# Performance work log

Measured on AMD Instinct MI355X. Metric: run time of the kernel, lower is better.

Reference implementation:

```python
import jax, jax.numpy as jnp
import numpy as np

N_HEAD = 16
D_MODEL = 1024
HEAD_DIM = D_MODEL // N_HEAD
B, S = 2, 2048


def setup_inputs() -> dict:
    key = jax.random.key(0)
    ks = jax.random.split(key, 7)
    qry = jax.random.normal(ks[0], (B, S, D_MODEL), dtype=jnp.float32)
    k_in = jax.random.normal(ks[1], (B, S, D_MODEL), dtype=jnp.float32)
    v_in = jax.random.normal(ks[2], (B, S, D_MODEL), dtype=jnp.float32)
    # causal boolean mask (B, S_q, S_k) as asserted in SelfAttention.forward
    attn_mask = jnp.broadcast_to(jnp.tril(jnp.ones((S, S), dtype=bool)), (B, S, S))
    scale = 1.0 / np.sqrt(D_MODEL)
    Wq = jax.random.normal(ks[3], (D_MODEL, D_MODEL), dtype=jnp.float32) * scale
    Wk = jax.random.normal(ks[4], (D_MODEL, D_MODEL), dtype=jnp.float32) * scale
    Wv = jax.random.normal(ks[5], (D_MODEL, D_MODEL), dtype=jnp.float32) * scale
    Wo = jax.random.normal(ks[6], (D_MODEL, D_MODEL), dtype=jnp.float32) * scale
    return {"qry": qry, "key": k_in, "val": v_in, "attn_mask": attn_mask,
            "Wq": Wq, "Wk": Wk, "Wv": Wv, "Wo": Wo}


def reference(qry, key, val, attn_mask, Wq, Wk, Wv, Wo):
    Bq, Sq, _ = qry.shape
    # torch Linear: y = x @ W.T (no bias)
    q = (qry @ Wq.T).reshape(Bq, Sq, N_HEAD, HEAD_DIM).transpose(0, 2, 1, 3)
    k = (key @ Wk.T).reshape(Bq, -1, N_HEAD, HEAD_DIM).transpose(0, 2, 1, 3)
    v = (val @ Wv.T).reshape(Bq, -1, N_HEAD, HEAD_DIM).transpose(0, 2, 1, 3)
    # scores: [B, H, Sq, Sk]
    scores = jnp.einsum('bhqd,bhkd->bhqk', q, k) / jnp.sqrt(jnp.float32(HEAD_DIM * N_HEAD) / N_HEAD)
    # attn_bias: 0 where mask True, -inf where False; broadcast over heads
    bias = jnp.where(attn_mask[:, None, :, :], 0.0, -jnp.inf).astype(scores.dtype)
    attn_weights = jax.nn.softmax(scores + bias, axis=-1)
    attn_feats = jnp.einsum('bhqk,bhkd->bhqd', attn_weights, v)
    attn_feats = attn_feats.transpose(0, 2, 1, 3).reshape(Bq, Sq, D_MODEL)
    output = attn_feats @ Wo.T
    return output, attn_weights
```

## Files before the change

### kernel.cpp

```cpp
#include <hip/hip_runtime.h>
#include <hip/hip_bf16.h>
#include <cstdint>
#include <cstddef>

#define DM 1024
#define NH 16
#define HD 64
#define BB 2
#define SS 2048

typedef __attribute__((ext_vector_type(4))) float f32x4;
typedef __attribute__((ext_vector_type(8))) short bf16x8;

typedef __attribute__((address_space(1))) const void GV;
typedef __attribute__((address_space(3))) void LV;

__global__ __launch_bounds__(256) void cvt_all(
    const float* s0, const float* s1, const float* s2, const float* s3,
    const float* s4, const float* s5, const float* s6,
    __hip_bfloat16* d0, __hip_bfloat16* d1, __hip_bfloat16* d2, __hip_bfloat16* d3,
    __hip_bfloat16* d4, __hip_bfloat16* d5, __hip_bfloat16* d6) {
    const float* s; __hip_bfloat16* d; int n4;
    switch (blockIdx.y) {
        case 0: s = s0; d = d0; n4 = 1 << 20; break;
        case 1: s = s1; d = d1; n4 = 1 << 20; break;
        case 2: s = s2; d = d2; n4 = 1 << 20; break;
        case 3: s = s3; d = d3; n4 = 1 << 18; break;
        case 4: s = s4; d = d4; n4 = 1 << 18; break;
        case 5: s = s5; d = d5; n4 = 1 << 18; break;
        default: s = s6; d = d6; n4 = 1 << 18; break;
    }
    for (int i = blockIdx.x * 256 + threadIdx.x; i < n4; i += 1024 * 256) {
        float4 v = reinterpret_cast<const float4*>(s)[i];
        ushort4 o;
        o.x = __builtin_bit_cast(unsigned short, __float2bfloat16(v.x));
        o.y = __builtin_bit_cast(unsigned short, __float2bfloat16(v.y));
        o.z = __builtin_bit_cast(unsigned short, __float2bfloat16(v.z));
        o.w = __builtin_bit_cast(unsigned short, __float2bfloat16(v.w));
        reinterpret_cast<ushort4*>(d)[i] = o;
    }
}

template <typename OutT>
__device__ __forceinline__ void gemm_body(const __hip_bfloat16* __restrict__ A,
                                          const __hip_bfloat16* __restrict__ Bw,
                                          OutT* __restrict__ C, int M, int N, int K,
                                          float alpha,
                                          __hip_bfloat16* As, __hip_bfloat16* Bs) {
    const int lane = threadIdx.x & 63;
    const int wv = threadIdx.x >> 6;
    const int wr = wv >> 1, wc = wv & 1;
    const int g = lane >> 4, cq = lane & 15;
    const int tM = blockIdx.y * 128, tN = blockIdx.x * 128;

    f32x4 acc[4][4];
#pragma unroll
    for (int i = 0; i < 4; ++i)
#pragma unroll
        for (int j = 0; j < 4; ++j) acc[i][j] = (f32x4){0.f, 0.f, 0.f, 0.f};

    for (int k0 = 0; k0 < K; k0 += 32) {
        __syncthreads();
#pragma unroll
        for (int r = 0; r < 2; ++r) {
            int chunk = r * 256 + wv * 64 + lane;
            int row = chunk >> 2;
            int kk = (chunk & 3) * 8;
            __builtin_amdgcn_global_load_lds((GV*)(A + (size_t)(tM + row) * K + k0 + kk),
                                             (LV*)(As + (size_t)(r * 256 + wv * 64) * 8), 16, 0, 0);
            __builtin_amdgcn_global_load_lds((GV*)(Bw + (size_t)(tN + row) * K + k0 + kk),
                                             (LV*)(Bs + (size_t)(r * 256 + wv * 64) * 8), 16, 0, 0);
        }
        __syncthreads();

        bf16x8 af[4], bfr[4];
#pragma unroll
        for (int i = 0; i < 4; ++i)
            af[i] = *reinterpret_cast<const bf16x8*>(As + (wr * 64 + i * 16 + cq) * 32 + g * 8);
#pragma unroll
        for (int j = 0; j < 4; ++j)
            bfr[j] = *reinterpret_cast<const bf16x8*>(Bs + (wc * 64 + j * 16 + cq) * 32 + g * 8);
#pragma unroll
        for (int i = 0; i < 4; ++i)
#pragma unroll
            for (int j = 0; j < 4; ++j)
                acc[i][j] = __builtin_amdgcn_mfma_f32_16x16x32_bf16(af[i], bfr[j], acc[i][j], 0, 0, 0);
    }

#pragma unroll
    for (int i = 0; i < 4; ++i)
#pragma unroll
        for (int j = 0; j < 4; ++j)
#pragma unroll
            for (int rr = 0; rr < 4; ++rr) {
                int row = tM + wr * 64 + i * 16 + g * 4 + rr;
                int col = tN + wc * 64 + j * 16 + cq;
                float v = acc[i][j][rr] * alpha;
                if constexpr (__is_same(OutT, float)) {
                    C[(size_t)row * N + col] = v;
                } else {
                    C[(size_t)row * N + col] = __float2bfloat16(v);
                }
            }
}

#define QALPHA 0.1803368801111204f

__global__ __launch_bounds__(256) void gemm_qkv(
    const __hip_bfloat16* qa, const __hip_bfloat16* ka, const __hip_bfloat16* va,
    const __hip_bfloat16* wq, const __hip_bfloat16* wk, const __hip_bfloat16* wv,
    __hip_bfloat16* Qm, __hip_bfloat16* Km, __hip_bfloat16* Vm) {
    __shared__ __hip_bfloat16 As[128 * 32];
    __shared__ __hip_bfloat16 Bs[128 * 32];
    const __hip_bfloat16 *A, *Bw;
    __hip_bfloat16* C;
    float alpha = 1.0f;
    switch (blockIdx.z) {
        case 0: A = qa; Bw = wq; C = Qm; alpha = QALPHA; break;
        case 1: A = ka; Bw = wk; C = Km; break;
        default: A = va; Bw = wv; C = Vm; break;
    }
    gemm_body<__hip_bfloat16>(A, Bw, C, BB * SS, DM, DM, alpha, As, Bs);
}

__global__ __launch_bounds__(256) void gemm_out(const __hip_bfloat16* __restrict__ A,
                                                const __hip_bfloat16* __restrict__ Bw,
                                                float* __restrict__ C) {
    __shared__ __hip_bfloat16 As[128 * 32];
    __shared__ __hip_bfloat16 Bs[128 * 32];
    gemm_body<float>(A, Bw, C, BB * SS, DM, DM, 1.0f, As, Bs);
}

__global__ __launch_bounds__(256) void transpose_v(const __hip_bfloat16* __restrict__ V,
                                                   __hip_bfloat16* __restrict__ VT) {
    const int bh = blockIdx.x;
    const int b = bh >> 4, h = bh & 15;
    const int k0 = blockIdx.y * 64;
    __shared__ __hip_bfloat16 tile[64][65];
    const int r = threadIdx.x / 64;
    const int c = threadIdx.x % 64;
#pragma unroll
    for (int rr = r; rr < 64; rr += 4)
        tile[rr][c] = V[(size_t)(b * SS + k0 + rr) * DM + h * HD + c];
    __syncthreads();
#pragma unroll
    for (int rr = r; rr < 64; rr += 4)
        VT[((size_t)bh * HD + rr) * SS + k0 + c] = tile[c][rr];
}

__global__ __launch_bounds__(256) void attn_fused(const __hip_bfloat16* __restrict__ Q,
                                                  const __hip_bfloat16* __restrict__ Kb,
                                                  const __hip_bfloat16* __restrict__ VT,
                                                  float* __restrict__ Wout,
                                                  __hip_bfloat16* __restrict__ feats) {
    __shared__ __hip_bfloat16 klds[2][64][64];
    __shared__ __hip_bfloat16 vlds[2][64][64];
    __shared__ __hip_bfloat16 plds[4][16][64];
    const int qt = (SS / 64 - 1) - blockIdx.x;
    const int bh = blockIdx.y;
    const int b = bh >> 4, h = bh & 15;
    const int lane = threadIdx.x & 63;
    const int wv = threadIdx.x >> 6;
    const int g = lane >> 4, cq = lane & 15;
    const int q0w = qt * 64 + wv * 16;
    const size_t rowbase = (size_t)b * SS;
    const int tmaxw = q0w >> 4;

    const __hip_bfloat16* qp = Q + (rowbase + q0w + cq) * DM + h * HD + g * 8;
    const bf16x8 qf0 = *reinterpret_cast<const bf16x8*>(qp);
    const bf16x8 qf1 = *reinterpret_cast<const bf16x8*>(qp + 32);

    auto stageK = [&](int kc, int buf) {
#pragma unroll
        for (int i = 0; i < 2; ++i) {
            int slot = i * 256 + wv * 64 + lane;
            int row = slot >> 3, c16 = slot & 7;
            const __hip_bfloat16* src =
                Kb + (rowbase + kc * 64 + row) * DM + h * HD + ((c16 ^ (row & 7)) << 3);
            __builtin_amdgcn_global_load_lds(
                (GV*)src, (LV*)(&klds[buf][0][0] + (size_t)(i * 256 + wv * 64) * 8), 16, 0, 0);
        }
    };
    auto stageV = [&](int kc, int buf) {
#pragma unroll
        for (int i = 0; i < 2; ++i) {
            int slot = i * 256 + wv * 64 + lane;
            int row = slot >> 3, c16 = slot & 7;
            const __hip_bfloat16* src =
                VT + ((size_t)bh * HD + row) * SS + kc * 64 + ((c16 ^ (row & 7)) << 3);
            __builtin_amdgcn_global_load_lds(
                (GV*)src, (LV*)(&vlds[buf][0][0] + (size_t)(i * 256 + wv * 64) * 8), 16, 0, 0);
        }
    };

    const int swx = cq & 7;

    float l_[4] = {0.f, 0.f, 0.f, 0.f};
    stageK(0, 0);
    for (int kc = 0; kc <= qt; ++kc) {
        const int cur = kc & 1;
        __syncthreads();
        if (kc < qt) stageK(kc + 1, cur ^ 1);
#pragma unroll
        for (int hh = 0; hh < 4; ++hh) {
            const int kt = kc * 4 + hh;
            if (kt > tmaxw) break;
            const __hip_bfloat16* kb = &klds[cur][hh * 16 + cq][0];
            bf16x8 kf0 = *reinterpret_cast<const bf16x8*>(kb + ((g ^ swx) << 3));
            bf16x8 kf1 = *reinterpret_cast<const bf16x8*>(kb + (((4 + g) ^ swx) << 3));
            f32x4 sc = (f32x4){0.f, 0.f, 0.f, 0.f};
            sc = __builtin_amdgcn_mfma_f32_16x16x32_bf16(qf0, kf0, sc, 0, 0, 0);
            sc = __builtin_amdgcn_mfma_f32_16x16x32_bf16(qf1, kf1, sc, 0, 0, 0);
            const int kk = kt * 16 + cq;
#pragma unroll
            for (int r = 0; r < 4; ++r) {
                const int qr = q0w + g * 4 + r;
                float p = (kk <= qr) ? __builtin_amdgcn_exp2f(sc[r]) : 0.0f;
                l_[r] += p;
            }
        }
    }
    float invl[4];
#pragma unroll
    for (int r = 0; r < 4; ++r) {
        float l = l_[r];
#pragma unroll
        for (int mk = 1; mk < 16; mk <<= 1) l += __shfl_xor(l, mk);
        invl[r] = __builtin_amdgcn_rcpf(l);
    }

    f32x4 oacc[4];
#pragma unroll
    for (int j = 0; j < 4; ++j) oacc[j] = (f32x4){0.f, 0.f, 0.f, 0.f};

    __syncthreads();
    stageK(0, 0);
    stageV(0, 0);
    for (int kc = 0; kc <= qt; ++kc) {
        const int cur = kc & 1;
        __syncthreads();
        if (kc < qt) { stageK(kc + 1, cur ^ 1); stageV(kc + 1, cur ^ 1); }

#pragma unroll
        for (int hh = 0; hh < 4; ++hh) {
            const int kt = kc * 4 + hh;
            if (kt <= tmaxw) {
                const __hip_bfloat16* kb = &klds[cur][hh * 16 + cq][0];
                bf16x8 kf0 = *reinterpret_cast<const bf16x8*>(kb + ((g ^ swx) << 3));
                bf16x8 kf1 = *reinterpret_cast<const bf16x8*>(kb + (((4 + g) ^ swx) << 3));
                f32x4 sc = (f32x4){0.f, 0.f, 0.f, 0.f};
                sc = __builtin_amdgcn_mfma_f32_16x16x32_bf16(qf0, kf0, sc, 0, 0, 0);
                sc = __builtin_amdgcn_mfma_f32_16x16x32_bf16(qf1, kf1, sc, 0, 0, 0);
                const int kk = kt * 16 + cq;
#pragma unroll
                for (int r = 0; r < 4; ++r) {
                    const int row = g * 4 + r;
                    const int qr = q0w + row;
                    float w = (kk <= qr) ? __builtin_amdgcn_exp2f(sc[r]) * invl[r] : 0.0f;
                    plds[wv][row][(hh * 16 + cq) ^ (8 * (row & 7))] = __float2bfloat16(w);
                }
            } else {
#pragma unroll
                for (int r = 0; r < 4; ++r) {
                    const int row = g * 4 + r;
                    plds[wv][row][(hh * 16 + cq) ^ (8 * (row & 7))] = __float2bfloat16(0.0f);
                }
            }
        }

        const int sw = 8 * swx;
        bf16x8 wa0 = *reinterpret_cast<const bf16x8*>(&plds[wv][cq][(g * 8) ^ sw]);
        bf16x8 wa1 = *reinterpret_cast<const bf16x8*>(&plds[wv][cq][(32 + g * 8) ^ sw]);
        __builtin_amdgcn_s_setprio(1);
#pragma unroll
        for (int j = 0; j < 4; ++j) {
            const __hip_bfloat16* vb = &vlds[cur][j * 16 + cq][0];
            bf16x8 vb0 = *reinterpret_cast<const bf16x8*>(vb + ((g ^ swx) << 3));
            bf16x8 vb1 = *reinterpret_cast<const bf16x8*>(vb + (((4 + g) ^ swx) << 3));
            oacc[j] = __builtin_amdgcn_mfma_f32_16x16x32_bf16(wa0, vb0, oacc[j], 0, 0, 0);
            oacc[j] = __builtin_amdgcn_mfma_f32_16x16x32_bf16(wa1, vb1, oacc[j], 0, 0, 0);
        }
        __builtin_amdgcn_s_setprio(0);

#pragma unroll
        for (int rh = 0; rh < 2; ++rh)
#pragma unroll
            for (int ch = 0; ch < 2; ++ch) {
                const int row = rh * 8 + (lane >> 3);
                const int fc = ch * 32 + (lane & 7) * 4;
                ushort4 u = *reinterpret_cast<const ushort4*>(
                    &plds[wv][row][fc ^ (8 * (row & 7))]);
                f32x4 v4;
                v4[0] = __builtin_bit_cast(float, (uint32_t)u.x << 16);
                v4[1] = __builtin_bit_cast(float, (uint32_t)u.y << 16);
                v4[2] = __builtin_bit_cast(float, (uint32_t)u.z << 16);
                v4[3] = __builtin_bit_cast(float, (uint32_t)u.w << 16);
                __builtin_nontemporal_store(
                    v4, reinterpret_cast<f32x4*>(
                            Wout + ((size_t)bh * SS + q0w + row) * SS + kc * 64 + fc));
            }
    }

    const int zstart = (qt + 1) * 64;
    const f32x4 z4 = (f32x4){0.f, 0.f, 0.f, 0.f};
    const int zrow = lane >> 2;
    const int zc = (lane & 3) * 4;
    for (int c = zstart; c < SS; c += 64) {
#pragma unroll
        for (int it = 0; it < 4; ++it) {
            f32x4* p = reinterpret_cast<f32x4*>(
                Wout + ((size_t)bh * SS + q0w + zrow) * SS + c + it * 16 + zc);
            __builtin_nontemporal_store(z4, p);
        }
    }

#pragma unroll
    for (int j = 0; j < 4; ++j)
#pragma unroll
        for (int r = 0; r < 4; ++r)
            feats[(rowbase + q0w + g * 4 + r) * DM + h * HD + j * 16 + cq] =
                __float2bfloat16(oacc[j][r]);
}

extern "C" void kernel_launch(void* const* d_in, const int* in_sizes, int n_in,
                              void* d_out, int out_size, void* d_ws, size_t ws_size,
                              hipStream_t stream) {
    (void)in_sizes; (void)n_in; (void)out_size;
    const float* qry = (const float*)d_in[0];
    const float* key = (const float*)d_in[1];
    const float* val = (const float*)d_in[2];
    const float* Wq = (const float*)d_in[4];
    const float* Wk = (const float*)d_in[5];
    const float* Wv = (const float*)d_in[6];
    const float* Wo = (const float*)d_in[7];

    float* out = (float*)d_out;
    float* w_out = out + (size_t)BB * SS * DM;

    const size_t E = (size_t)BB * SS * DM;
    const size_t W = (size_t)DM * DM;
    if (ws_size < (8 * E + 4 * W) * sizeof(__hip_bfloat16)) return;

    __hip_bfloat16* ws = (__hip_bfloat16*)d_ws;
    __hip_bfloat16* qb    = ws;
    __hip_bfloat16* kb    = ws + E;
    __hip_bfloat16* vb    = ws + 2 * E;
    __hip_bfloat16* wqb   = ws + 3 * E;
    __hip_bfloat16* wkb   = ws + 3 * E + W;
    __hip_bfloat16* wvb   = ws + 3 * E + 2 * W;
    __hip_bfloat16* wob   = ws + 3 * E + 3 * W;
    __hip_bfloat16* Qm    = ws + 3 * E + 4 * W;
    __hip_bfloat16* Km    = ws + 4 * E + 4 * W;
    __hip_bfloat16* Vm    = ws + 5 * E + 4 * W;
    __hip_bfloat16* VTm   = ws + 6 * E + 4 * W;
    __hip_bfloat16* feats = ws + 7 * E + 4 * W;

    cvt_all<<<dim3(1024, 7), 256, 0, stream>>>(qry, key, val, Wq, Wk, Wv, Wo,
                                               qb, kb, vb, wqb, wkb, wvb, wob);

    gemm_qkv<<<dim3(DM / 128, (BB * SS) / 128, 3), 256, 0, stream>>>(
        qb, kb, vb, wqb, wkb, wvb, Qm, Km, Vm);

    transpose_v<<<dim3(BB * NH, SS / 64), 256, 0, stream>>>(Vm, VTm);

    attn_fused<<<dim3(SS / 64, BB * NH), 256, 0, stream>>>(Qm, Km, VTm, w_out, feats);

    gemm_out<<<dim3(DM / 128, (BB * SS) / 128), 256, 0, stream>>>(feats, wob, out);
}
```

Measured before the change: 284.5 us.

## Fuse V transpose into QKV GEMM epilogue and restructure attention weight writes

The V projection GEMM now writes its output directly in transposed per-head layout, which removes the separate transpose kernel and its extra round trip through global memory. The attention kernel swaps the MFMA operands so that each lane holds four consecutive key scores for one query row. This lets the probabilities go straight from registers to the fp32 weight output as vector stores instead of being bounced through LDS, and it cuts the row-sum reduction to two shuffles. The launch becomes a 1D grid with a remapped order that spreads heavy causal tiles across blocks, and bf16 packing now uses v_cvt_pk_bf16_f32. The tradeoff is that the epilogue stores in the V GEMM become scattered, and the weight stores are 16-byte per lane rather than fully coalesced rows.

```diff
diff --git a/kernel.cpp b/kernel.cpp
--- a/kernel.cpp
+++ b/kernel.cpp
@@ -11,9 +11,16 @@
 
 typedef __attribute__((ext_vector_type(4))) float f32x4;
 typedef __attribute__((ext_vector_type(8))) short bf16x8;
+typedef __attribute__((ext_vector_type(2))) unsigned int u32x2;
 
 typedef __attribute__((address_space(1))) const void GV;
 typedef __attribute__((address_space(3))) void LV;
+
+__device__ __forceinline__ uint32_t cvtpk_bf16(float lo, float hi) {
+    uint32_t r;
+    asm("v_cvt_pk_bf16_f32 %0, %1, %2" : "=v"(r) : "v"(lo), "v"(hi));
+    return r;
+}
 
 __global__ __launch_bounds__(256) void cvt_all(
     const float* s0, const float* s1, const float* s2, const float* s3,
@@ -41,11 +48,10 @@
     }
 }
 
-template <typename OutT>
+template <int MODE>
 __device__ __forceinline__ void gemm_body(const __hip_bfloat16* __restrict__ A,
                                           const __hip_bfloat16* __restrict__ Bw,
-                                          OutT* __restrict__ C, int M, int N, int K,
-                                          float alpha,
+                                          void* __restrict__ Cv, float alpha,
                                           __hip_bfloat16* As, __hip_bfloat16* Bs) {
     const int lane = threadIdx.x & 63;
     const int wv = threadIdx.x >> 6;
@@ -59,16 +65,16 @@
 #pragma unroll
         for (int j = 0; j < 4; ++j) acc[i][j] = (f32x4){0.f, 0.f, 0.f, 0.f};
 
-    for (int k0 = 0; k0 < K; k0 += 32) {
+    for (int k0 = 0; k0 < DM; k0 += 32) {
         __syncthreads();
 #pragma unroll
         for (int r = 0; r < 2; ++r) {
             int chunk = r * 256 + wv * 64 + lane;
             int row = chunk >> 2;
             int kk = (chunk & 3) * 8;
-            __builtin_amdgcn_global_load_lds((GV*)(A + (size_t)(tM + row) * K + k0 + kk),
+            __builtin_amdgcn_global_load_lds((GV*)(A + (size_t)(tM + row) * DM + k0 + kk),
                                              (LV*)(As + (size_t)(r * 256 + wv * 64) * 8), 16, 0, 0);
-            __builtin_amdgcn_global_load_lds((GV*)(Bw + (size_t)(tN + row) * K + k0 + kk),
+            __builtin_amdgcn_global_load_lds((GV*)(Bw + (size_t)(tN + row) * DM + k0 + kk),
                                              (LV*)(Bs + (size_t)(r * 256 + wv * 64) * 8), 16, 0, 0);
         }
         __syncthreads();
@@ -90,18 +96,33 @@
 #pragma unroll
     for (int i = 0; i < 4; ++i)
 #pragma unroll
-        for (int j = 0; j < 4; ++j)
-#pragma unroll
-            for (int rr = 0; rr < 4; ++rr) {
-                int row = tM + wr * 64 + i * 16 + g * 4 + rr;
+        for (int j = 0; j < 4; ++j) {
+            if constexpr (MODE == 2) {
+                __hip_bfloat16* VTo = (__hip_bfloat16*)Cv;
+                int row0 = tM + wr * 64 + i * 16 + g * 4;
                 int col = tN + wc * 64 + j * 16 + cq;
-                float v = acc[i][j][rr] * alpha;
-                if constexpr (__is_same(OutT, float)) {
-                    C[(size_t)row * N + col] = v;
-                } else {
-                    C[(size_t)row * N + col] = __float2bfloat16(v);
+                int b = row0 >> 11, s = row0 & (SS - 1);
+                size_t off = ((size_t)((b << 4) + (col >> 6)) * HD + (col & 63)) * SS + s;
+                ushort4 o;
+                o.x = __builtin_bit_cast(unsigned short, __float2bfloat16(acc[i][j][0]));
+                o.y = __builtin_bit_cast(unsigned short, __float2bfloat16(acc[i][j][1]));
+                o.z = __builtin_bit_cast(unsigned short, __float2bfloat16(acc[i][j][2]));
+                o.w = __builtin_bit_cast(unsigned short, __float2bfloat16(acc[i][j][3]));
+                *reinterpret_cast<ushort4*>(VTo + off) = o;
+            } else {
+#pragma unroll
+                for (int rr = 0; rr < 4; ++rr) {
+                    int row = tM + wr * 64 + i * 16 + g * 4 + rr;
+                    int col = tN + wc * 64 + j * 16 + cq;
+                    float v = acc[i][j][rr] * alpha;
+                    if constexpr (MODE == 1) {
+                        ((float*)Cv)[(size_t)row * DM + col] = v;
+                    } else {
+                        ((__hip_bfloat16*)Cv)[(size_t)row * DM + col] = __float2bfloat16(v);
+                    }
                 }
             }
+        }
 }
 
 #define QALPHA 0.1803368801111204f
@@ -109,18 +130,16 @@
 __global__ __launch_bounds__(256) void gemm_qkv(
     const __hip_bfloat16* qa, const __hip_bfloat16* ka, const __hip_bfloat16* va,
     const __hip_bfloat16* wq, const __hip_bfloat16* wk, const __hip_bfloat16* wv,
-    __hip_bfloat16* Qm, __hip_bfloat16* Km, __hip_bfloat16* Vm) {
+    __hip_bfloat16* Qm, __hip_bfloat16* Km, __hip_bfloat16* VTm) {
     __shared__ __hip_bfloat16 As[128 * 32];
     __shared__ __hip_bfloat16 Bs[128 * 32];
-    const __hip_bfloat16 *A, *Bw;
-    __hip_bfloat16* C;
-    float alpha = 1.0f;
-    switch (blockIdx.z) {
-        case 0: A = qa; Bw = wq; C = Qm; alpha = QALPHA; break;
-        case 1: A = ka; Bw = wk; C = Km; break;
-        default: A = va; Bw = wv; C = Vm; break;
-    }
-    gemm_body<__hip_bfloat16>(A, Bw, C, BB * SS, DM, DM, alpha, As, Bs);
+    if (blockIdx.z == 0) {
+        gemm_body<0>(qa, wq, Qm, QALPHA, As, Bs);
+    } else if (blockIdx.z == 1) {
+        gemm_body<0>(ka, wk, Km, 1.0f, As, Bs);
+    } else {
+        gemm_body<2>(va, wv, VTm, 1.0f, As, Bs);
+    }
 }
 
 __global__ __launch_bounds__(256) void gemm_out(const __hip_bfloat16* __restrict__ A,
@@ -128,24 +147,7 @@
                                                 float* __restrict__ C) {
     __shared__ __hip_bfloat16 As[128 * 32];
     __shared__ __hip_bfloat16 Bs[128 * 32];
-    gemm_body<float>(A, Bw, C, BB * SS, DM, DM, 1.0f, As, Bs);
-}
-
-__global__ __launch_bounds__(256) void transpose_v(const __hip_bfloat16* __restrict__ V,
-                                                   __hip_bfloat16* __restrict__ VT) {
-    const int bh = blockIdx.x;
-    const int b = bh >> 4, h = bh & 15;
-    const int k0 = blockIdx.y * 64;
-    __shared__ __hip_bfloat16 tile[64][65];
-    const int r = threadIdx.x / 64;
-    const int c = threadIdx.x % 64;
-#pragma unroll
-    for (int rr = r; rr < 64; rr += 4)
-        tile[rr][c] = V[(size_t)(b * SS + k0 + rr) * DM + h * HD + c];
-    __syncthreads();
-#pragma unroll
-    for (int rr = r; rr < 64; rr += 4)
-        VT[((size_t)bh * HD + rr) * SS + k0 + c] = tile[c][rr];
+    gemm_body<1>(A, Bw, C, 1.0f, As, Bs);
 }
 
 __global__ __launch_bounds__(256) void attn_fused(const __hip_bfloat16* __restrict__ Q,
@@ -156,8 +158,9 @@
     __shared__ __hip_bfloat16 klds[2][64][64];
     __shared__ __hip_bfloat16 vlds[2][64][64];
     __shared__ __hip_bfloat16 plds[4][16][64];
-    const int qt = (SS / 64 - 1) - blockIdx.x;
-    const int bh = blockIdx.y;
+    const int v = (blockIdx.x & 7) * 128 + (blockIdx.x >> 3);
+    const int bh = v >> 5;
+    const int qt = 31 - (v & 31);
     const int b = bh >> 4, h = bh & 15;
     const int lane = threadIdx.x & 63;
     const int wv = threadIdx.x >> 6;
@@ -165,8 +168,10 @@
     const int q0w = qt * 64 + wv * 16;
     const size_t rowbase = (size_t)b * SS;
     const int tmaxw = q0w >> 4;
-
-    const __hip_bfloat16* qp = Q + (rowbase + q0w + cq) * DM + h * HD + g * 8;
+    const int qrow = q0w + cq;
+    const int swx = cq & 7;
+
+    const __hip_bfloat16* qp = Q + (rowbase + qrow) * DM + h * HD + g * 8;
     const bf16x8 qf0 = *reinterpret_cast<const bf16x8*>(qp);
     const bf16x8 qf1 = *reinterpret_cast<const bf16x8*>(qp + 32);
 
@@ -193,9 +198,7 @@
         }
     };
 
-    const int swx = cq & 7;
-
-    float l_[4] = {0.f, 0.f, 0.f, 0.f};
+    float l = 0.f;
     stageK(0, 0);
     for (int kc = 0; kc <= qt; ++kc) {
         const int cur = kc & 1;
@@ -209,25 +212,17 @@
             bf16x8 kf0 = *reinterpret_cast<const bf16x8*>(kb + ((g ^ swx) << 3));
             bf16x8 kf1 = *reinterpret_cast<const bf16x8*>(kb + (((4 + g) ^ swx) << 3));
             f32x4 sc = (f32x4){0.f, 0.f, 0.f, 0.f};
-            sc = __builtin_amdgcn_mfma_f32_16x16x32_bf16(qf0, kf0, sc, 0, 0, 0);
-            sc = __builtin_amdgcn_mfma_f32_16x16x32_bf16(qf1, kf1, sc, 0, 0, 0);
-            const int kk = kt * 16 + cq;
-#pragma unroll
-            for (int r = 0; r < 4; ++r) {
-                const int qr = q0w + g * 4 + r;
-                float p = (kk <= qr) ? __builtin_amdgcn_exp2f(sc[r]) : 0.0f;
-                l_[r] += p;
-            }
-        }
-    }
-    float invl[4];
-#pragma unroll
-    for (int r = 0; r < 4; ++r) {
-        float l = l_[r];
-#pragma unroll
-        for (int mk = 1; mk < 16; mk <<= 1) l += __shfl_xor(l, mk);
-        invl[r] = __builtin_amdgcn_rcpf(l);
-    }
+            sc = __builtin_amdgcn_mfma_f32_16x16x32_bf16(kf0, qf0, sc, 0, 0, 0);
+            sc = __builtin_amdgcn_mfma_f32_16x16x32_bf16(kf1, qf1, sc, 0, 0, 0);
+            const int k0 = kt * 16 + g * 4;
+#pragma unroll
+            for (int r = 0; r < 4; ++r)
+                l += (k0 + r <= qrow) ? __builtin_amdgcn_exp2f(sc[r]) : 0.0f;
+        }
+    }
+    l += __shfl_xor(l, 16);
+    l += __shfl_xor(l, 32);
+    const float invl = __builtin_amdgcn_rcpf(l);
 
     f32x4 oacc[4];
 #pragma unroll
@@ -241,78 +236,55 @@
         __syncthreads();
         if (kc < qt) { stageK(kc + 1, cur ^ 1); stageV(kc + 1, cur ^ 1); }
 
+        const bool active = (kc * 4 <= tmaxw);
 #pragma unroll
         for (int hh = 0; hh < 4; ++hh) {
             const int kt = kc * 4 + hh;
+            const int k0 = kt * 16 + g * 4;
+            f32x4 wn = (f32x4){0.f, 0.f, 0.f, 0.f};
             if (kt <= tmaxw) {
                 const __hip_bfloat16* kb = &klds[cur][hh * 16 + cq][0];
                 bf16x8 kf0 = *reinterpret_cast<const bf16x8*>(kb + ((g ^ swx) << 3));
                 bf16x8 kf1 = *reinterpret_cast<const bf16x8*>(kb + (((4 + g) ^ swx) << 3));
                 f32x4 sc = (f32x4){0.f, 0.f, 0.f, 0.f};
-                sc = __builtin_amdgcn_mfma_f32_16x16x32_bf16(qf0, kf0, sc, 0, 0, 0);
-                sc = __builtin_amdgcn_mfma_f32_16x16x32_bf16(qf1, kf1, sc, 0, 0, 0);
-                const int kk = kt * 16 + cq;
-#pragma unroll
-                for (int r = 0; r < 4; ++r) {
-                    const int row = g * 4 + r;
-                    const int qr = q0w + row;
-                    float w = (kk <= qr) ? __builtin_amdgcn_exp2f(sc[r]) * invl[r] : 0.0f;
-                    plds[wv][row][(hh * 16 + cq) ^ (8 * (row & 7))] = __float2bfloat16(w);
-                }
-            } else {
-#pragma unroll
-                for (int r = 0; r < 4; ++r) {
-                    const int row = g * 4 + r;
-                    plds[wv][row][(hh * 16 + cq) ^ (8 * (row & 7))] = __float2bfloat16(0.0f);
-                }
+                sc = __builtin_amdgcn_mfma_f32_16x16x32_bf16(kf0, qf0, sc, 0, 0, 0);
+                sc = __builtin_amdgcn_mfma_f32_16x16x32_bf16(kf1, qf1, sc, 0, 0, 0);
+#pragma unroll
+                for (int r = 0; r < 4; ++r)
+                    wn[r] = (k0 + r <= qrow) ? __builtin_amdgcn_exp2f(sc[r]) * invl : 0.0f;
             }
-        }
-
-        const int sw = 8 * swx;
-        bf16x8 wa0 = *reinterpret_cast<const bf16x8*>(&plds[wv][cq][(g * 8) ^ sw]);
-        bf16x8 wa1 = *reinterpret_cast<const bf16x8*>(&plds[wv][cq][(32 + g * 8) ^ sw]);
-        __builtin_amdgcn_s_setprio(1);
-#pragma unroll
-        for (int j = 0; j < 4; ++j) {
-            const __hip_bfloat16* vb = &vlds[cur][j * 16 + cq][0];
-            bf16x8 vb0 = *reinterpret_cast<const bf16x8*>(vb + ((g ^ swx) << 3));
-            bf16x8 vb1 = *reinterpret_cast<const bf16x8*>(vb + (((4 + g) ^ swx) << 3));
-            oacc[j] = __builtin_amdgcn_mfma_f32_16x16x32_bf16(wa0, vb0, oacc[j], 0, 0, 0);
-            oacc[j] = __builtin_amdgcn_mfma_f32_16x16x32_bf16(wa1, vb1, oacc[j], 0, 0, 0);
-        }
-        __builtin_amdgcn_s_setprio(0);
-
-#pragma unroll
-        for (int rh = 0; rh < 2; ++rh)
-#pragma unroll
-            for (int ch = 0; ch < 2; ++ch) {
-                const int row = rh * 8 + (lane >> 3);
-                const int fc = ch * 32 + (lane & 7) * 4;
-                ushort4 u = *reinterpret_cast<const ushort4*>(
-                    &plds[wv][row][fc ^ (8 * (row & 7))]);
-                f32x4 v4;
-                v4[0] = __builtin_bit_cast(float, (uint32_t)u.x << 16);
-                v4[1] = __builtin_bit_cast(float, (uint32_t)u.y << 16);
-                v4[2] = __builtin_bit_cast(float, (uint32_t)u.z << 16);
-                v4[3] = __builtin_bit_cast(float, (uint32_t)u.w << 16);
-                __builtin_nontemporal_store(
-                    v4, reinterpret_cast<f32x4*>(
-                            Wout + ((size_t)bh * SS + q0w + row) * SS + kc * 64 + fc));
+            __builtin_nontemporal_store(
+                wn, reinterpret_cast<f32x4*>(Wout + ((size_t)bh * SS + qrow) * SS + k0));
+            if (active) {
+                u32x2 uu;
+                uu[0] = cvtpk_bf16(wn[0], wn[1]);
+                uu[1] = cvtpk_bf16(wn[2], wn[3]);
+                const int gran = (hh * 2 + (g >> 1)) ^ swx;
+                *reinterpret_cast<u32x2*>(&plds[wv][cq][gran * 8 + (g & 1) * 4]) = uu;
             }
+        }
+
+        if (active) {
+            bf16x8 wa0 = *reinterpret_cast<const bf16x8*>(&plds[wv][cq][(g ^ swx) * 8]);
+            bf16x8 wa1 = *reinterpret_cast<const bf16x8*>(&plds[wv][cq][((4 + g) ^ swx) * 8]);
+            __builtin_amdgcn_s_setprio(1);
+#pragma unroll
+            for (int j = 0; j < 4; ++j) {
+                const __hip_bfloat16* vb = &vlds[cur][j * 16 + cq][0];
+                bf16x8 vb0 = *reinterpret_cast<const bf16x8*>(vb + ((g ^ swx) << 3));
+                bf16x8 vb1 = *reinterpret_cast<const bf16x8*>(vb + (((4 + g) ^ swx) << 3));
+                oacc[j] = __builtin_amdgcn_mfma_f32_16x16x32_bf16(wa0, vb0, oacc[j], 0, 0, 0);
+                oacc[j] = __builtin_amdgcn_mfma_f32_16x16x32_bf16(wa1, vb1, oacc[j], 0, 0, 0);
+            }
+            __builtin_amdgcn_s_setprio(0);
+        }
     }
 
     const int zstart = (qt + 1) * 64;
     const f32x4 z4 = (f32x4){0.f, 0.f, 0.f, 0.f};
-    const int zrow = lane >> 2;
-    const int zc = (lane & 3) * 4;
-    for (int c = zstart; c < SS; c += 64) {
-#pragma unroll
-        for (int it = 0; it < 4; ++it) {
-            f32x4* p = reinterpret_cast<f32x4*>(
-                Wout + ((size_t)bh * SS + q0w + zrow) * SS + c + it * 16 + zc);
-            __builtin_nontemporal_store(z4, p);
-        }
-    }
+    for (int c = zstart + g * 16; c < SS; c += 64)
+        __builtin_nontemporal_store(
+            z4, reinterpret_cast<f32x4*>(Wout + ((size_t)bh * SS + qrow) * SS + c));
 
 #pragma unroll
     for (int j = 0; j < 4; ++j)
@@ -351,19 +323,16 @@
     __hip_bfloat16* wob   = ws + 3 * E + 3 * W;
     __hip_bfloat16* Qm    = ws + 3 * E + 4 * W;
     __hip_bfloat16* Km    = ws + 4 * E + 4 * W;
-    __hip_bfloat16* Vm    = ws + 5 * E + 4 * W;
-    __hip_bfloat16* VTm   = ws + 6 * E + 4 * W;
-    __hip_bfloat16* feats = ws + 7 * E + 4 * W;
+    __hip_bfloat16* VTm   = ws + 5 * E + 4 * W;
+    __hip_bfloat16* feats = ws + 6 * E + 4 * W;
 
     cvt_all<<<dim3(1024, 7), 256, 0, stream>>>(qry, key, val, Wq, Wk, Wv, Wo,
                                                qb, kb, vb, wqb, wkb, wvb, wob);
 
     gemm_qkv<<<dim3(DM / 128, (BB * SS) / 128, 3), 256, 0, stream>>>(
-        qb, kb, vb, wqb, wkb, wvb, Qm, Km, Vm);
-
-    transpose_v<<<dim3(BB * NH, SS / 64), 256, 0, stream>>>(Vm, VTm);
-
-    attn_fused<<<dim3(SS / 64, BB * NH), 256, 0, stream>>>(Qm, Km, VTm, w_out, feats);
+        qb, kb, vb, wqb, wkb, wvb, Qm, Km, VTm);
+
+    attn_fused<<<dim3(1024), 256, 0, stream>>>(Qm, Km, VTm, w_out, feats);
 
     gemm_out<<<dim3(DM / 128, (BB * SS) / 128), 256, 0, stream>>>(feats, wob, out);
 }
```

Result: slower. 367.0 us (+29.0%).
